# Kernel tuning notes

Hardware: AMD Instinct MI355X
Metric: run time of the kernel (lower is better)

Reference implementation:

```python
import jax, jax.numpy as jnp
import numpy as np

NE, NR, D, H, L = 200000, 500, 128, 4, 2
HD = D // H
N, E, B = 32768, 262144, 256
MARGIN = 1.0


def setup_inputs() -> dict:
    key = jax.random.key(0)
    ks = jax.random.split(key, 16)
    nrm = lambda k, shp, s=0.05: jax.random.normal(k, shp, jnp.float32) * s
    inp = {
        'ent_emb': nrm(ks[0], (NE, D)),
        'rel_emb': nrm(ks[1], (NR, D)),
        'rel_prior': nrm(ks[2], (NR, 1)),
    }
    for i, nm in enumerate(['Wq', 'Wk', 'Wv', 'Wo', 'Wek', 'Wev']):
        inp[nm] = nrm(ks[3 + i], (L, D, D))
    for gi, g in enumerate(['h', 't', 'n']):
        kb = jax.random.fold_in(key, 100 + gi)
        k1, k2, k3, k4 = jax.random.split(kb, 4)
        inp[f'x_{g}'] = jax.random.randint(k1, (N,), 0, NE, jnp.int32)
        inp[f'ei_{g}'] = jax.random.randint(k2, (2, E), 0, N, jnp.int32)
        inp[f'ea_{g}'] = jax.random.randint(k3, (E,), 0, NR, jnp.int32)
        inp[f'y_{g}'] = jax.random.randint(k4, (B,), 0, N // B, jnp.int32)
        inp[f's_{g}'] = jnp.full((B,), N // B, dtype=jnp.int32)
    inp['sample'] = jax.random.randint(ks[9], (B, 3), 0, NR, jnp.int32)
    return inp


def gnn_embed(ent_emb, rel_emb, rel_prior, Wq, Wk, Wv, Wo, Wek, Wev, x, ei, ea, y, s):
    n = x.shape[0]
    h = ent_emb[x]                    # [N, D] node features (embedding lookup)
    e_emb = rel_emb[ea]               # [E, D] edge relation embedding
    e_pri = rel_prior[ea]             # [E, 1] scalar relation prior gate
    src, dst = ei[0], ei[1]
    scale = 1.0 / np.sqrt(HD).astype(np.float32)
    for l in range(L):
        q = (h @ Wq[l]).reshape(n, H, HD)[dst]                               # [E,H,HD]
        k = (h @ Wk[l]).reshape(n, H, HD)[src] + (e_emb @ Wek[l]).reshape(-1, H, HD)
        v = (h @ Wv[l]).reshape(n, H, HD)[src] + (e_emb @ Wev[l]).reshape(-1, H, HD)
        score = jnp.sum(q * k, axis=-1) * scale * e_pri                      # [E,H]
        # segment softmax over incoming edges of each destination node
        m = jax.ops.segment_max(score, dst, num_segments=n)
        m = jnp.where(jnp.isfinite(m), m, 0.0)
        ex = jnp.exp(score - m[dst])
        den = jax.ops.segment_sum(ex, dst, num_segments=n)[dst]
        alpha = ex / (den + 1e-16)                                           # [E,H]
        msg = jax.ops.segment_sum((alpha[..., None] * v).reshape(-1, D), dst, num_segments=n)
        h = jax.nn.gelu(h + msg @ Wo[l])                                     # residual + activation
    # get_real_index: exclusive cumsum of graph sizes + local target index
    offsets = jnp.concatenate([jnp.zeros((1,), s.dtype), jnp.cumsum(s)[:-1]])
    return h[offsets + y]             # [B, D]


def reference(ent_emb, rel_emb, rel_prior, Wq, Wk, Wv, Wo, Wek, Wev,
              x_h, ei_h, ea_h, y_h, s_h,
              x_t, ei_t, ea_t, y_t, s_t,
              x_n, ei_n, ea_n, y_n, s_n, sample):
    g = lambda x, ei, ea, y, s: gnn_embed(ent_emb, rel_emb, rel_prior, Wq, Wk, Wv, Wo, Wek, Wev, x, ei, ea, y, s)
    h = g(x_h, ei_h, ea_h, y_h, s_h)[:, None, :]   # [B,1,D]
    t = g(x_t, ei_t, ea_t, y_t, s_t)[:, None, :]
    tn = g(x_n, ei_n, ea_n, y_n, s_n)[:, None, :]
    r = rel_emb[sample[:, 1]][:, None, :]          # [B,1,D]
    proj_t = h + r                                 # TransE projection
    pos = jnp.linalg.norm(t - proj_t + 1e-8, axis=2)   # [B,1]
    negs = jnp.linalg.norm(t - tn + 1e-8, axis=2)      # [B,1]
    neg = jnp.mean(negs, axis=-1)                      # [B]
    # MarginRankingLoss(pos, neg, target=-1): mean(max(0, (pos-neg)+margin)); broadcasts [B,1]-[B] -> [B,B]
    loss = jnp.mean(jnp.maximum(pos - neg + MARGIN, 0.0))
    return loss
```

## Files before the change

kernel.cpp:

```cpp
#include <hip/hip_runtime.h>
#include <hip/hip_bf16.h>
#include <math.h>

#define NEC 200000
#define NRC 500
#define DD 128
#define LLC 2
#define NNODE 32768
#define EEDGE 262144
#define BBATCH 256
#define NG 3
#define BCAP 32
#define NSB 32
#define EPG (EEDGE / NSB)
#define CNTW (NNODE / 4)

typedef __attribute__((ext_vector_type(8))) short short8;
typedef __attribute__((ext_vector_type(4))) float floatx4;
typedef __attribute__((ext_vector_type(2))) float floatx2;

__device__ __forceinline__ float bf2f(unsigned short u) {
  union { unsigned int i; float f; } c; c.i = ((unsigned int)u) << 16; return c.f;
}
__device__ __forceinline__ unsigned short f2bf(float f) {
  union { float f; unsigned int i; } c; c.f = f;
  unsigned int x = c.i;
  unsigned int r = x + 0x7fffu + ((x >> 16) & 1u);
  return (unsigned short)(r >> 16);
}
__device__ __forceinline__ float bfu_lo(unsigned int u) {
  union { unsigned int i; float f; } c; c.i = u << 16; return c.f;
}
__device__ __forceinline__ float bfu_hi(unsigned int u) {
  union { unsigned int i; float f; } c; c.i = u & 0xffff0000u; return c.f;
}

__device__ __forceinline__ bool detect_fm(const void* ent) {
  unsigned int u = ((const unsigned int*)ent)[threadIdx.x & 63];
  bool big = fabsf(bfu_lo(u)) > 100.f;
  return __ballot(big) != 0ull;
}

__global__ __launch_bounds__(128) void k_prep(const void* ent, const void* rel,
    const void* prior, const void* Wq, const void* Wk, const void* Wv, const void* Wo,
    const void* Wek, const void* Wev,
    float* pris, unsigned short* WT, unsigned short* relk, unsigned short* relv) {
  bool fm = detect_fm(ent);
  int bid = blockIdx.x, tid = threadIdx.x;
  if (bid < 4) {
    int r = bid * 128 + tid;
    if (r < NRC) {
      float p = fm ? ((const float*)prior)[r] : bf2f(((const unsigned short*)prior)[r]);
      pris[r] = p * 0.17677669529663687f;
    }
  } else if (bid < 1028) {
    int t = (bid - 4) * 128 + tid;
    int mat = t >> 15;
    int rem = t & 32767;
    int l = rem >> 14;
    int p = rem & 16383;
    int d = p >> 7, c = p & 127;
    const void* W = mat == 0 ? Wq : (mat == 1 ? Wk : (mat == 2 ? Wv : Wo));
    size_t src = (size_t)l * DD * DD + (size_t)c * DD + d;
    float v = fm ? ((const float*)W)[src] : bf2f(((const unsigned short*)W)[src]);
    WT[(((size_t)mat * LLC + l) * DD + d) * DD + c] = f2bf(v);
  } else {
    int rid = bid - 1028;
    int which = rid / 1000;
    int l = (rid / 500) % 2;
    int r = rid % 500;
    int d = tid;
    size_t wofs = (size_t)l * DD * DD;
    const float* Wf = (const float*)(which ? Wev : Wek) + wofs;
    const unsigned short* Wb = (const unsigned short*)(which ? Wev : Wek) + wofs;
    __shared__ float re[DD];
    re[d] = fm ? ((const float*)rel)[r * DD + d] : bf2f(((const unsigned short*)rel)[r * DD + d]);
    __syncthreads();
    float acc = 0.f;
    if (fm) { for (int c = 0; c < DD; ++c) acc += re[c] * Wf[c * DD + d]; }
    else    { for (int c = 0; c < DD; ++c) acc += re[c] * bf2f(Wb[c * DD + d]); }
    unsigned short* out = which ? relv : relk;
    out[((size_t)l * NRC + r) * DD + d] = f2bf(acc);
  }
}

__global__ __launch_bounds__(256) void k_gather(const void* ent,
    const int* x0, const int* x1, const int* x2, unsigned short* hbf) {
  bool fm = detect_fm(ent);
  int bid = blockIdx.x, tid = threadIdx.x;
  int rbase = bid * 64;
  int g = rbase >> 15;
  const int* x = g == 0 ? x0 : (g == 1 ? x1 : x2);
  int c = tid & 31;
  int j8 = tid >> 5;
  int rows[8], xs[8];
  #pragma unroll
  for (int k = 0; k < 8; ++k) {
    rows[k] = rbase + j8 + 8 * k;
    xs[k] = x[rows[k] & (NNODE - 1)];
  }
  if (fm) {
    float4 v[8];
    #pragma unroll
    for (int k = 0; k < 8; ++k)
      v[k] = *reinterpret_cast<const float4*>((const float*)ent + (size_t)xs[k] * DD + c * 4);
    #pragma unroll
    for (int k = 0; k < 8; ++k) {
      uint2 o;
      o.x = ((unsigned int)f2bf(v[k].y) << 16) | (unsigned int)f2bf(v[k].x);
      o.y = ((unsigned int)f2bf(v[k].w) << 16) | (unsigned int)f2bf(v[k].z);
      *reinterpret_cast<uint2*>(hbf + (size_t)rows[k] * DD + c * 4) = o;
    }
  } else {
    uint2 v[8];
    #pragma unroll
    for (int k = 0; k < 8; ++k)
      v[k] = *reinterpret_cast<const uint2*>((const unsigned short*)ent + (size_t)xs[k] * DD + c * 4);
    #pragma unroll
    for (int k = 0; k < 8; ++k)
      *reinterpret_cast<uint2*>(hbf + (size_t)rows[k] * DD + c * 4) = v[k];
  }
}

__global__ __launch_bounds__(1024) void k_count(const int* ei0, const int* ei1,
    const int* ei2, unsigned int* cntw) {
  __shared__ unsigned int cnt[CNTW];
  int bid = blockIdx.x, tid = threadIdx.x;
  int g = bid / NSB, grp = bid % NSB;
  const int* ei = g == 0 ? ei0 : (g == 1 ? ei1 : ei2);
  #pragma unroll
  for (int i = 0; i < CNTW / 1024; ++i) cnt[i * 1024 + tid] = 0u;
  __syncthreads();
  int e0 = grp * EPG;
  #pragma unroll
  for (int i = 0; i < EPG / 1024; ++i) {
    int dst = ei[EEDGE + e0 + i * 1024 + tid];
    atomicAdd(&cnt[dst >> 2], 1u << ((dst & 3) * 8));
  }
  __syncthreads();
  unsigned int* out = cntw + (size_t)(g * NSB + grp) * CNTW;
  #pragma unroll
  for (int i = 0; i < CNTW / 1024; ++i) out[i * 1024 + tid] = cnt[i * 1024 + tid];
}

__global__ __launch_bounds__(256) void k_prefix(const unsigned int* cntw,
    unsigned int* basew, int* deg) {
  int flat = blockIdx.x * 256 + threadIdx.x;
  int g = flat / CNTW, wi = flat % CNTW;
  unsigned int r0 = 0, r1 = 0, r2 = 0, r3 = 0;
  for (int grp = 0; grp < NSB; ++grp) {
    size_t idx = (size_t)(g * NSB + grp) * CNTW + wi;
    unsigned int w = cntw[idx];
    basew[idx] = r0 | (r1 << 8) | (r2 << 16) | (r3 << 24);
    r0 += w & 255u; r1 += (w >> 8) & 255u; r2 += (w >> 16) & 255u; r3 += (w >> 24) & 255u;
  }
  int4 dv = {(int)r0, (int)r1, (int)r2, (int)r3};
  *reinterpret_cast<int4*>(deg + (size_t)g * NNODE + wi * 4) = dv;
}

__global__ __launch_bounds__(1024) void k_place(const int* ei0, const int* ei1,
    const int* ei2, const int* ea0, const int* ea1, const int* ea2,
    const unsigned int* basew, unsigned int* bucket) {
  __shared__ unsigned int cnt[CNTW];
  __shared__ unsigned int basel[CNTW];
  int bid = blockIdx.x, tid = threadIdx.x;
  int g = bid / NSB, grp = bid % NSB;
  const int* ei = g == 0 ? ei0 : (g == 1 ? ei1 : ei2);
  const int* ea = g == 0 ? ea0 : (g == 1 ? ea1 : ea2);
  const unsigned int* brow = basew + (size_t)(g * NSB + grp) * CNTW;
  #pragma unroll
  for (int i = 0; i < CNTW / 1024; ++i) {
    cnt[i * 1024 + tid] = 0u;
    basel[i * 1024 + tid] = brow[i * 1024 + tid];
  }
  __syncthreads();
  int e0 = grp * EPG;
  size_t gb = (size_t)g * NNODE;
  #pragma unroll
  for (int i = 0; i < EPG / 1024; ++i) {
    int e = e0 + i * 1024 + tid;
    int dst = ei[EEDGE + e];
    unsigned int src = (unsigned int)ei[e];
    unsigned int r = (unsigned int)ea[e];
    int sh = (dst & 3) * 8;
    unsigned int old = atomicAdd(&cnt[dst >> 2], 1u << sh);
    unsigned int lpos = (old >> sh) & 255u;
    unsigned int b = (basel[dst >> 2] >> sh) & 255u;
    unsigned int slot = b + lpos;
    if (slot < BCAP)
      bucket[(gb + dst) * BCAP + slot] = src | (r << 15);
  }
}

__device__ __forceinline__ void stage_wt(const unsigned short* WT, int tid,
                                         unsigned short (*Wt)[136]) {
  #pragma unroll
  for (int pass = 0; pass < 8; ++pass) {
    int idx = pass * 256 + tid;
    int d = idx >> 4, c0 = (idx & 15) << 3;
    *reinterpret_cast<short8*>(&Wt[d][c0]) =
        *reinterpret_cast<const short8*>(WT + d * DD + c0);
  }
}

__global__ __launch_bounds__(256) void k_gemm_qkv(const unsigned short* A,
    const unsigned short* WT, int layer, unsigned short* Qo, unsigned char* KV) {
  __shared__ unsigned short Wt[DD][136];
  int g = blockIdx.y;
  const unsigned short* Ag = A + (size_t)g * NNODE * DD;
  int tid = threadIdx.x;
  int w = tid >> 6, lane = tid & 63;
  int m = lane & 15, quad = lane >> 4;
  int row = blockIdx.x * 64 + w * 16 + m;
  int rowbase = blockIdx.x * 64;
  const unsigned short* arow = Ag + (size_t)row * DD;
  short8 a[4];
  #pragma unroll
  for (int ks = 0; ks < 4; ++ks)
    a[ks] = *reinterpret_cast<const short8*>(arow + ks * 32 + quad * 8);

  for (int mat = 0; mat < 3; ++mat) {
    if (mat) __syncthreads();
    stage_wt(WT + ((size_t)mat * LLC + layer) * DD * DD, tid, Wt);
    __syncthreads();
    floatx4 acc[8];
    #pragma unroll
    for (int t = 0; t < 8; ++t) acc[t] = (floatx4){0.f, 0.f, 0.f, 0.f};
    #pragma unroll
    for (int ks = 0; ks < 4; ++ks) {
      #pragma unroll
      for (int t = 0; t < 8; ++t) {
        short8 b = *reinterpret_cast<const short8*>(&Wt[t * 16 + m][ks * 32 + quad * 8]);
        acc[t] = __builtin_amdgcn_mfma_f32_16x16x32_bf16(a[ks], b, acc[t], 0, 0, 0);
      }
    }
    __syncthreads();
    unsigned short* ut = &Wt[0][0];
    #pragma unroll
    for (int t = 0; t < 8; ++t) {
      #pragma unroll
      for (int r = 0; r < 4; ++r) {
        ut[(w * 16 + quad * 4 + r) * 136 + t * 16 + m] = f2bf(acc[t][r]);
      }
    }
    __syncthreads();
    if (mat == 0) {
      unsigned short* Og = Qo + (size_t)g * NNODE * DD;
      #pragma unroll
      for (int k = 0; k < 4; ++k) {
        int flat = k * 256 + tid;
        int rw = flat >> 4, c8 = flat & 15;
        short8 v = *reinterpret_cast<const short8*>(ut + rw * 136 + c8 * 8);
        *reinterpret_cast<short8*>(Og + (size_t)(rowbase + rw) * DD + c8 * 8) = v;
      }
    } else {
      unsigned char* kvb = KV + (size_t)g * NNODE * 256 + (mat == 1 ? 0 : 128);
      #pragma unroll
      for (int k = 0; k < 2; ++k) {
        int flat = k * 256 + tid;
        int rw = flat >> 3, c16 = flat & 7;
        const unsigned short* p = ut + rw * 136 + c16 * 16;
        uint4 va = *reinterpret_cast<const uint4*>(p);
        uint4 vb = *reinterpret_cast<const uint4*>(p + 8);
        unsigned int w0 = __builtin_amdgcn_cvt_pk_fp8_f32(bfu_lo(va.x), bfu_hi(va.x), 0u, false);
        w0 = __builtin_amdgcn_cvt_pk_fp8_f32(bfu_lo(va.y), bfu_hi(va.y), w0, true);
        unsigned int w1 = __builtin_amdgcn_cvt_pk_fp8_f32(bfu_lo(va.z), bfu_hi(va.z), 0u, false);
        w1 = __builtin_amdgcn_cvt_pk_fp8_f32(bfu_lo(va.w), bfu_hi(va.w), w1, true);
        unsigned int w2 = __builtin_amdgcn_cvt_pk_fp8_f32(bfu_lo(vb.x), bfu_hi(vb.x), 0u, false);
        w2 = __builtin_amdgcn_cvt_pk_fp8_f32(bfu_lo(vb.y), bfu_hi(vb.y), w2, true);
        unsigned int w3 = __builtin_amdgcn_cvt_pk_fp8_f32(bfu_lo(vb.z), bfu_hi(vb.z), 0u, false);
        w3 = __builtin_amdgcn_cvt_pk_fp8_f32(bfu_lo(vb.w), bfu_hi(vb.w), w3, true);
        uint4 o = {w0, w1, w2, w3};
        *reinterpret_cast<uint4*>(kvb + (size_t)(rowbase + rw) * 256 + c16 * 16) = o;
      }
    }
  }
}

__global__ __launch_bounds__(256) void k_gemm_o(const unsigned short* A,
    const unsigned short* WT, int layer, unsigned short* hbf) {
  __shared__ unsigned short Wt[DD][136];
  int g = blockIdx.y;
  const unsigned short* Ag = A + (size_t)g * NNODE * DD;
  unsigned short* hbg = hbf + (size_t)g * NNODE * DD;
  int tid = threadIdx.x;
  stage_wt(WT + ((size_t)3 * LLC + layer) * DD * DD, tid, Wt);
  __syncthreads();
  int w = tid >> 6, lane = tid & 63;
  int m = lane & 15, quad = lane >> 4;
  int row = blockIdx.x * 64 + w * 16 + m;
  floatx4 acc[8];
  #pragma unroll
  for (int t = 0; t < 8; ++t) acc[t] = (floatx4){0.f, 0.f, 0.f, 0.f};
  const unsigned short* arow = Ag + (size_t)row * DD;
  #pragma unroll
  for (int ks = 0; ks < 4; ++ks) {
    short8 a = *reinterpret_cast<const short8*>(arow + ks * 32 + quad * 8);
    #pragma unroll
    for (int t = 0; t < 8; ++t) {
      short8 b = *reinterpret_cast<const short8*>(&Wt[t * 16 + m][ks * 32 + quad * 8]);
      acc[t] = __builtin_amdgcn_mfma_f32_16x16x32_bf16(a, b, acc[t], 0, 0, 0);
    }
  }
  __syncthreads();
  float* ft = (float*)&Wt[0][0];
  #pragma unroll
  for (int t = 0; t < 8; ++t) {
    #pragma unroll
    for (int r = 0; r < 4; ++r) {
      ft[(w * 16 + quad * 4 + r) * 136 + t * 16 + m] = acc[t][r];
    }
  }
  __syncthreads();
  int rowbase = blockIdx.x * 64;
  #pragma unroll
  for (int k = 0; k < 8; ++k) {
    int flat = k * 256 + tid;
    int rw = flat >> 5, c4 = flat & 31;
    float4 v = *reinterpret_cast<const float4*>(ft + rw * 136 + c4 * 4);
    size_t gi = (size_t)(rowbase + rw) * DD + c4 * 4;
    uint2 hv = *reinterpret_cast<const uint2*>(hbg + gi);
    float h0 = bfu_lo(hv.x), h1 = bfu_hi(hv.x), h2 = bfu_lo(hv.y), h3 = bfu_hi(hv.y);
    float r0, r1, r2, r3;
    {
      float xv = v.x + h0;
      float z2 = 1.5957691216057308f * (xv + 0.044715f * xv * xv * xv);
      r0 = xv / (1.f + __expf(-z2));
      xv = v.y + h1;
      z2 = 1.5957691216057308f * (xv + 0.044715f * xv * xv * xv);
      r1 = xv / (1.f + __expf(-z2));
      xv = v.z + h2;
      z2 = 1.5957691216057308f * (xv + 0.044715f * xv * xv * xv);
      r2 = xv / (1.f + __expf(-z2));
      xv = v.w + h3;
      z2 = 1.5957691216057308f * (xv + 0.044715f * xv * xv * xv);
      r3 = xv / (1.f + __expf(-z2));
    }
    uint2 o;
    o.x = ((unsigned int)f2bf(r1) << 16) | (unsigned int)f2bf(r0);
    o.y = ((unsigned int)f2bf(r3) << 16) | (unsigned int)f2bf(r2);
    *reinterpret_cast<uint2*>(hbg + gi) = o;
  }
}

__global__ __launch_bounds__(256) void k_attn(const unsigned short* Q, const unsigned char* KV,
    const unsigned short* relk, const unsigned short* relv,
    const float* pris, const int* deg, const unsigned int* bucket, int layer,
    unsigned short* msgb) {
  int w = threadIdx.x >> 6, lane = threadIdx.x & 63;
  int sq = lane >> 4;
  int sl = lane & 15;
  int g = blockIdx.y;
  int dst = blockIdx.x * 4 + w;
  const unsigned short* rk = relk + (size_t)layer * NRC * DD;
  const unsigned short* rv = relv + (size_t)layer * NRC * DD;
  const unsigned char* KVg = KV + (size_t)g * NNODE * 256;
  size_t gofs = (size_t)g * NNODE * DD;

  uint4 qu = *reinterpret_cast<const uint4*>(Q + gofs + (size_t)dst * DD + sl * 8);
  floatx2 q01 = {bfu_lo(qu.x), bfu_hi(qu.x)};
  floatx2 q23 = {bfu_lo(qu.y), bfu_hi(qu.y)};
  floatx2 q45 = {bfu_lo(qu.z), bfu_hi(qu.z)};
  floatx2 q67 = {bfu_lo(qu.w), bfu_hi(qu.w)};

  float den = 0.f;
  floatx2 m01 = {0.f, 0.f}, m23 = {0.f, 0.f}, m45 = {0.f, 0.f}, m67 = {0.f, 0.f};
  int dg = deg[g * NNODE + dst]; if (dg > BCAP) dg = BCAP;
  size_t base = ((size_t)g * NNODE + dst) * BCAP;
  if (dg > 0) {
    int niter = (dg + 3) >> 2;
    int e1 = 4 + sq; if (e1 >= dg) e1 = dg - 1;
    unsigned int pe_nxt = bucket[base + (sq < dg ? sq : dg - 1)];
    unsigned int pe_fut = bucket[base + e1];
    int src = (int)(pe_nxt & 32767u);
    int r = (int)(pe_nxt >> 15);
    const unsigned char* kvrow = KVg + (size_t)src * 256;
    uint2 k8 = *reinterpret_cast<const uint2*>(kvrow + sl * 8);
    uint2 v8 = *reinterpret_cast<const uint2*>(kvrow + 128 + sl * 8);
    uint4 rku = *reinterpret_cast<const uint4*>(rk + (size_t)r * DD + sl * 8);
    uint4 rvu = *reinterpret_cast<const uint4*>(rv + (size_t)r * DD + sl * 8);
    float p = pris[r];
    pe_nxt = pe_fut;
    for (int i = 0; i < niter; ++i) {
      int ef = 4 * (i + 2) + sq; if (ef >= dg) ef = dg - 1;
      pe_fut = bucket[base + ef];
      int nsrc = (int)(pe_nxt & 32767u);
      int nr = (int)(pe_nxt >> 15);
      const unsigned char* nkv = KVg + (size_t)nsrc * 256;
      uint2 nk8 = *reinterpret_cast<const uint2*>(nkv + sl * 8);
      uint2 nv8 = *reinterpret_cast<const uint2*>(nkv + 128 + sl * 8);
      uint4 nrku = *reinterpret_cast<const uint4*>(rk + (size_t)nr * DD + sl * 8);
      uint4 nrvu = *reinterpret_cast<const uint4*>(rv + (size_t)nr * DD + sl * 8);
      float np = pris[nr];
      floatx2 kk01 = __builtin_amdgcn_cvt_pk_f32_fp8(k8.x, false);
      floatx2 kk23 = __builtin_amdgcn_cvt_pk_f32_fp8(k8.x, true);
      floatx2 kk45 = __builtin_amdgcn_cvt_pk_f32_fp8(k8.y, false);
      floatx2 kk67 = __builtin_amdgcn_cvt_pk_f32_fp8(k8.y, true);
      floatx2 rk01 = {bfu_lo(rku.x), bfu_hi(rku.x)};
      floatx2 rk23 = {bfu_lo(rku.y), bfu_hi(rku.y)};
      floatx2 rk45 = {bfu_lo(rku.z), bfu_hi(rku.z)};
      floatx2 rk67 = {bfu_lo(rku.w), bfu_hi(rku.w)};
      floatx2 sv = (kk01 + rk01) * q01;
      sv += (kk23 + rk23) * q23;
      sv += (kk45 + rk45) * q45;
      sv += (kk67 + rk67) * q67;
      float s = sv.x + sv.y;
      s += __shfl_xor(s, 1); s += __shfl_xor(s, 2);
      bool valid = (4 * i + sq) < dg;
      float ex = valid ? __expf(s * p) : 0.f;
      floatx2 vv01 = __builtin_amdgcn_cvt_pk_f32_fp8(v8.x, false);
      floatx2 vv23 = __builtin_amdgcn_cvt_pk_f32_fp8(v8.x, true);
      floatx2 vv45 = __builtin_amdgcn_cvt_pk_f32_fp8(v8.y, false);
      floatx2 vv67 = __builtin_amdgcn_cvt_pk_f32_fp8(v8.y, true);
      floatx2 rv01 = {bfu_lo(rvu.x), bfu_hi(rvu.x)};
      floatx2 rv23 = {bfu_lo(rvu.y), bfu_hi(rvu.y)};
      floatx2 rv45 = {bfu_lo(rvu.z), bfu_hi(rvu.z)};
      floatx2 rv67 = {bfu_lo(rvu.w), bfu_hi(rvu.w)};
      floatx2 ex2 = {ex, ex};
      den += ex;
      m01 += ex2 * (vv01 + rv01);
      m23 += ex2 * (vv23 + rv23);
      m45 += ex2 * (vv45 + rv45);
      m67 += ex2 * (vv67 + rv67);
      k8 = nk8; v8 = nv8; rku = nrku; rvu = nrvu; p = np;
      pe_nxt = pe_fut;
    }
  }
  den += __shfl_xor(den, 16); den += __shfl_xor(den, 32);
  m01.x += __shfl_xor(m01.x, 16); m01.x += __shfl_xor(m01.x, 32);
  m01.y += __shfl_xor(m01.y, 16); m01.y += __shfl_xor(m01.y, 32);
  m23.x += __shfl_xor(m23.x, 16); m23.x += __shfl_xor(m23.x, 32);
  m23.y += __shfl_xor(m23.y, 16); m23.y += __shfl_xor(m23.y, 32);
  m45.x += __shfl_xor(m45.x, 16); m45.x += __shfl_xor(m45.x, 32);
  m45.y += __shfl_xor(m45.y, 16); m45.y += __shfl_xor(m45.y, 32);
  m67.x += __shfl_xor(m67.x, 16); m67.x += __shfl_xor(m67.x, 32);
  m67.y += __shfl_xor(m67.y, 16); m67.y += __shfl_xor(m67.y, 32);
  float inv = 1.f / (den + 1e-16f);
  if (sq == 0) {
    uint4 o;
    o.x = ((unsigned int)f2bf(m01.y * inv) << 16) | (unsigned int)f2bf(m01.x * inv);
    o.y = ((unsigned int)f2bf(m23.y * inv) << 16) | (unsigned int)f2bf(m23.x * inv);
    o.z = ((unsigned int)f2bf(m45.y * inv) << 16) | (unsigned int)f2bf(m45.x * inv);
    o.w = ((unsigned int)f2bf(m67.y * inv) << 16) | (unsigned int)f2bf(m67.x * inv);
    *reinterpret_cast<uint4*>(msgb + gofs + (size_t)dst * DD + sl * 8) = o;
  }
}

__global__ __launch_bounds__(128) void k_ep(const unsigned short* hbf, const void* ent,
    const void* rel,
    const int* y0, const int* s0, const int* y1, const int* s1, const int* y2, const int* s2,
    const int* sample, float* pos, float* neg) {
  bool fm = detect_fm(ent);
  int b = blockIdx.x, d = threadIdx.x;
  int oh = 0, ot = 0, on = 0;
  for (int j = 0; j < b; ++j) { oh += s0[j]; ot += s1[j]; on += s2[j]; }
  int ih = oh + y0[b], it = ot + y1[b], in_ = on + y2[b];
  float th = bf2f(hbf[((size_t)0 * NNODE + ih) * DD + d]);
  float tt = bf2f(hbf[((size_t)1 * NNODE + it) * DD + d]);
  float tn = bf2f(hbf[((size_t)2 * NNODE + in_) * DD + d]);
  int r = sample[b * 3 + 1];
  float rr = fm ? ((const float*)rel)[r * DD + d] : bf2f(((const unsigned short*)rel)[r * DD + d]);
  float dp = tt - (th + rr) + 1e-8f;
  float dn = tt - tn + 1e-8f;
  float ap = dp * dp, an = dn * dn;
  for (int o = 32; o > 0; o >>= 1) { ap += __shfl_down(ap, o); an += __shfl_down(an, o); }
  __shared__ float sa[2], sb[2];
  if ((d & 63) == 0) { sa[d >> 6] = ap; sb[d >> 6] = an; }
  __syncthreads();
  if (d == 0) { pos[b] = sqrtf(sa[0] + sa[1]); neg[b] = sqrtf(sb[0] + sb[1]); }
}

__global__ __launch_bounds__(256) void k_hinge(const float* pos, const float* neg,
    const void* ent, void* out) {
  bool fm = detect_fm(ent);
  __shared__ float ns[BBATCH];
  __shared__ float wsum[4];
  int t = threadIdx.x;
  ns[t] = neg[t];
  float pb = pos[t];
  __syncthreads();
  float local = 0.f;
  for (int j = 0; j < BBATCH; ++j) {
    float v = pb - ns[j] + 1.0f;
    local += v > 0.f ? v : 0.f;
  }
  for (int o = 32; o > 0; o >>= 1) local += __shfl_down(local, o);
  if ((t & 63) == 0) wsum[t >> 6] = local;
  __syncthreads();
  if (t == 0) {
    float loss = (wsum[0] + wsum[1] + wsum[2] + wsum[3]) * (1.f / (256.f * 256.f));
    if (fm) ((float*)out)[0] = loss;
    else    ((unsigned short*)out)[0] = f2bf(loss);
  }
}

extern "C" void kernel_launch(void* const* d_in, const int* in_sizes, int n_in,
                              void* d_out, int out_size, void* d_ws, size_t ws_size,
                              hipStream_t stream) {
  const void* ent   = d_in[0];
  const void* rel   = d_in[1];
  const void* prior = d_in[2];
  const void* Wq  = d_in[3];
  const void* Wk  = d_in[4];
  const void* Wv  = d_in[5];
  const void* Wo  = d_in[6];
  const void* Wek = d_in[7];
  const void* Wev = d_in[8];
  const int* sample = (const int*)d_in[24];

  size_t off = 0;
  char* basep = (char*)d_ws;
  auto alloc = [&](size_t bytes) -> void* {
    void* r = basep + off;
    off = (off + bytes + 255) & ~(size_t)255;
    return r;
  };
  unsigned short* hbf  = (unsigned short*)alloc((size_t)NG * NNODE * DD * 2);
  unsigned short* Qb   = (unsigned short*)alloc((size_t)NG * NNODE * DD * 2);
  unsigned char*  KV   = (unsigned char*)alloc((size_t)NG * NNODE * 256);
  unsigned short* msgb = (unsigned short*)alloc((size_t)NG * NNODE * DD * 2);
  unsigned short* relk = (unsigned short*)alloc((size_t)LLC * NRC * DD * 2);
  unsigned short* relv = (unsigned short*)alloc((size_t)LLC * NRC * DD * 2);
  unsigned short* WT   = (unsigned short*)alloc((size_t)4 * LLC * DD * DD * 2);
  float* pris = (float*)alloc((size_t)NRC * 4);
  int*   deg  = (int*)alloc((size_t)NG * NNODE * 4);
  unsigned int* bucket = (unsigned int*)alloc((size_t)NG * NNODE * BCAP * 4);
  unsigned int* cntw   = (unsigned int*)alloc((size_t)NG * NSB * CNTW * 4);
  unsigned int* basew  = (unsigned int*)alloc((size_t)NG * NSB * CNTW * 4);
  float* pos  = (float*)alloc((size_t)BBATCH * 4);
  float* neg  = (float*)alloc((size_t)BBATCH * 4);

  const int* x0  = (const int*)d_in[9],  *x1 = (const int*)d_in[14], *x2 = (const int*)d_in[19];
  const int* ei0 = (const int*)d_in[10], *ei1 = (const int*)d_in[15], *ei2 = (const int*)d_in[20];
  const int* ea0 = (const int*)d_in[11], *ea1 = (const int*)d_in[16], *ea2 = (const int*)d_in[21];
  const int* y0  = (const int*)d_in[12], *y1 = (const int*)d_in[17], *y2 = (const int*)d_in[22];
  const int* s0  = (const int*)d_in[13], *s1 = (const int*)d_in[18], *s2 = (const int*)d_in[23];

  k_prep<<<3028, 128, 0, stream>>>(ent, rel, prior, Wq, Wk, Wv, Wo, Wek, Wev,
                                   pris, WT, relk, relv);
  k_gather<<<1536, 256, 0, stream>>>(ent, x0, x1, x2, hbf);
  k_count<<<NG * NSB, 1024, 0, stream>>>(ei0, ei1, ei2, cntw);
  k_prefix<<<NG * CNTW / 256, 256, 0, stream>>>(cntw, basew, deg);
  k_place<<<NG * NSB, 1024, 0, stream>>>(ei0, ei1, ei2, ea0, ea1, ea2, basew, bucket);
  for (int l = 0; l < LLC; ++l) {
    k_gemm_qkv<<<dim3(NNODE / 64, NG), 256, 0, stream>>>(hbf, WT, l, Qb, KV);
    k_attn<<<dim3(NNODE / 4, NG), 256, 0, stream>>>(Qb, KV, relk, relv, pris, deg, bucket, l, msgb);
    k_gemm_o<<<dim3(NNODE / 64, NG), 256, 0, stream>>>(msgb, WT, l, hbf);
  }
  k_ep<<<BBATCH, 128, 0, stream>>>(hbf, ent, rel, y0, s0, y1, s1, y2, s2, sample, pos, neg);
  k_hinge<<<1, BBATCH, 0, stream>>>(pos, neg, ent, d_out);
}
```

Measured before the change: 471.2 us.

## Process two destination nodes per wavefront with deeper gather prefetch in attention

The attention kernel now maps two destination nodes to each 64-lane wavefront (32 lanes each, two edges in flight per node) instead of one node across four edge slots. The grid is halved and the final cross-lane reduction drops one shuffle stage. The KV row prefetch is deepened to two edges ahead, with relation rows loaded one edge ahead. This targets lane waste for low-degree nodes (the average degree is 8) and aims to hide more gather latency. The cost is more loop iterations per node and extra registers for the prefetch pipeline, which may lower occupancy.

```diff
diff --git a/kernel.cpp b/kernel.cpp
--- a/kernel.cpp
+++ b/kernel.cpp
@@ -348,10 +348,11 @@
     const float* pris, const int* deg, const unsigned int* bucket, int layer,
     unsigned short* msgb) {
   int w = threadIdx.x >> 6, lane = threadIdx.x & 63;
-  int sq = lane >> 4;
+  int half = lane >> 5;
+  int hq = (lane >> 4) & 1;
   int sl = lane & 15;
   int g = blockIdx.y;
-  int dst = blockIdx.x * 4 + w;
+  int dst = blockIdx.x * 8 + w * 2 + half;
   const unsigned short* rk = relk + (size_t)layer * NRC * DD;
   const unsigned short* rv = relv + (size_t)layer * NRC * DD;
   const unsigned char* KVg = KV + (size_t)g * NNODE * 256;
@@ -368,75 +369,81 @@
   int dg = deg[g * NNODE + dst]; if (dg > BCAP) dg = BCAP;
   size_t base = ((size_t)g * NNODE + dst) * BCAP;
   if (dg > 0) {
-    int niter = (dg + 3) >> 2;
-    int e1 = 4 + sq; if (e1 >= dg) e1 = dg - 1;
-    unsigned int pe_nxt = bucket[base + (sq < dg ? sq : dg - 1)];
-    unsigned int pe_fut = bucket[base + e1];
-    int src = (int)(pe_nxt & 32767u);
-    int r = (int)(pe_nxt >> 15);
-    const unsigned char* kvrow = KVg + (size_t)src * 256;
-    uint2 k8 = *reinterpret_cast<const uint2*>(kvrow + sl * 8);
-    uint2 v8 = *reinterpret_cast<const uint2*>(kvrow + 128 + sl * 8);
-    uint4 rku = *reinterpret_cast<const uint4*>(rk + (size_t)r * DD + sl * 8);
-    uint4 rvu = *reinterpret_cast<const uint4*>(rv + (size_t)r * DD + sl * 8);
-    float p = pris[r];
-    pe_nxt = pe_fut;
+    int niter = (dg + 1) >> 1;
+    int e0i = hq < dg ? hq : dg - 1;
+    int e1i = 2 + hq; if (e1i >= dg) e1i = dg - 1;
+    int e2i = 4 + hq; if (e2i >= dg) e2i = dg - 1;
+    unsigned int w0 = bucket[base + e0i];
+    unsigned int w1 = bucket[base + e1i];
+    unsigned int w2 = bucket[base + e2i];
+    int sA = (int)(w0 & 32767u), rA = (int)(w0 >> 15);
+    const unsigned char* rowA = KVg + (size_t)sA * 256;
+    uint2 kA = *reinterpret_cast<const uint2*>(rowA + sl * 8);
+    uint2 vA = *reinterpret_cast<const uint2*>(rowA + 128 + sl * 8);
+    uint4 rkA = *reinterpret_cast<const uint4*>(rk + (size_t)rA * DD + sl * 8);
+    uint4 rvA = *reinterpret_cast<const uint4*>(rv + (size_t)rA * DD + sl * 8);
+    float pA = pris[rA];
+    int sB = (int)(w1 & 32767u);
+    const unsigned char* rowB = KVg + (size_t)sB * 256;
+    uint2 kB = *reinterpret_cast<const uint2*>(rowB + sl * 8);
+    uint2 vB = *reinterpret_cast<const uint2*>(rowB + 128 + sl * 8);
     for (int i = 0; i < niter; ++i) {
-      int ef = 4 * (i + 2) + sq; if (ef >= dg) ef = dg - 1;
-      pe_fut = bucket[base + ef];
-      int nsrc = (int)(pe_nxt & 32767u);
-      int nr = (int)(pe_nxt >> 15);
-      const unsigned char* nkv = KVg + (size_t)nsrc * 256;
-      uint2 nk8 = *reinterpret_cast<const uint2*>(nkv + sl * 8);
-      uint2 nv8 = *reinterpret_cast<const uint2*>(nkv + 128 + sl * 8);
-      uint4 nrku = *reinterpret_cast<const uint4*>(rk + (size_t)nr * DD + sl * 8);
-      uint4 nrvu = *reinterpret_cast<const uint4*>(rv + (size_t)nr * DD + sl * 8);
-      float np = pris[nr];
-      floatx2 kk01 = __builtin_amdgcn_cvt_pk_f32_fp8(k8.x, false);
-      floatx2 kk23 = __builtin_amdgcn_cvt_pk_f32_fp8(k8.x, true);
-      floatx2 kk45 = __builtin_amdgcn_cvt_pk_f32_fp8(k8.y, false);
-      floatx2 kk67 = __builtin_amdgcn_cvt_pk_f32_fp8(k8.y, true);
-      floatx2 rk01 = {bfu_lo(rku.x), bfu_hi(rku.x)};
-      floatx2 rk23 = {bfu_lo(rku.y), bfu_hi(rku.y)};
-      floatx2 rk45 = {bfu_lo(rku.z), bfu_hi(rku.z)};
-      floatx2 rk67 = {bfu_lo(rku.w), bfu_hi(rku.w)};
+      int e3 = 2 * (i + 3) + hq; if (e3 >= dg) e3 = dg - 1;
+      unsigned int w3 = bucket[base + e3];
+      int sC = (int)(w2 & 32767u);
+      const unsigned char* rowC = KVg + (size_t)sC * 256;
+      uint2 kC = *reinterpret_cast<const uint2*>(rowC + sl * 8);
+      uint2 vC = *reinterpret_cast<const uint2*>(rowC + 128 + sl * 8);
+      int rB = (int)(w1 >> 15);
+      uint4 rkB = *reinterpret_cast<const uint4*>(rk + (size_t)rB * DD + sl * 8);
+      uint4 rvB = *reinterpret_cast<const uint4*>(rv + (size_t)rB * DD + sl * 8);
+      float pB = pris[rB];
+      floatx2 kk01 = __builtin_amdgcn_cvt_pk_f32_fp8(kA.x, false);
+      floatx2 kk23 = __builtin_amdgcn_cvt_pk_f32_fp8(kA.x, true);
+      floatx2 kk45 = __builtin_amdgcn_cvt_pk_f32_fp8(kA.y, false);
+      floatx2 kk67 = __builtin_amdgcn_cvt_pk_f32_fp8(kA.y, true);
+      floatx2 rk01 = {bfu_lo(rkA.x), bfu_hi(rkA.x)};
+      floatx2 rk23 = {bfu_lo(rkA.y), bfu_hi(rkA.y)};
+      floatx2 rk45 = {bfu_lo(rkA.z), bfu_hi(rkA.z)};
+      floatx2 rk67 = {bfu_lo(rkA.w), bfu_hi(rkA.w)};
       floatx2 sv = (kk01 + rk01) * q01;
       sv += (kk23 + rk23) * q23;
       sv += (kk45 + rk45) * q45;
       sv += (kk67 + rk67) * q67;
       float s = sv.x + sv.y;
       s += __shfl_xor(s, 1); s += __shfl_xor(s, 2);
-      bool valid = (4 * i + sq) < dg;
-      float ex = valid ? __expf(s * p) : 0.f;
-      floatx2 vv01 = __builtin_amdgcn_cvt_pk_f32_fp8(v8.x, false);
-      floatx2 vv23 = __builtin_amdgcn_cvt_pk_f32_fp8(v8.x, true);
-      floatx2 vv45 = __builtin_amdgcn_cvt_pk_f32_fp8(v8.y, false);
-      floatx2 vv67 = __builtin_amdgcn_cvt_pk_f32_fp8(v8.y, true);
-      floatx2 rv01 = {bfu_lo(rvu.x), bfu_hi(rvu.x)};
-      floatx2 rv23 = {bfu_lo(rvu.y), bfu_hi(rvu.y)};
-      floatx2 rv45 = {bfu_lo(rvu.z), bfu_hi(rvu.z)};
-      floatx2 rv67 = {bfu_lo(rvu.w), bfu_hi(rvu.w)};
+      bool valid = (2 * i + hq) < dg;
+      float ex = valid ? __expf(s * pA) : 0.f;
+      floatx2 vv01 = __builtin_amdgcn_cvt_pk_f32_fp8(vA.x, false);
+      floatx2 vv23 = __builtin_amdgcn_cvt_pk_f32_fp8(vA.x, true);
+      floatx2 vv45 = __builtin_amdgcn_cvt_pk_f32_fp8(vA.y, false);
+      floatx2 vv67 = __builtin_amdgcn_cvt_pk_f32_fp8(vA.y, true);
+      floatx2 rv01 = {bfu_lo(rvA.x), bfu_hi(rvA.x)};
+      floatx2 rv23 = {bfu_lo(rvA.y), bfu_hi(rvA.y)};
+      floatx2 rv45 = {bfu_lo(rvA.z), bfu_hi(rvA.z)};
+      floatx2 rv67 = {bfu_lo(rvA.w), bfu_hi(rvA.w)};
       floatx2 ex2 = {ex, ex};
       den += ex;
       m01 += ex2 * (vv01 + rv01);
       m23 += ex2 * (vv23 + rv23);
       m45 += ex2 * (vv45 + rv45);
       m67 += ex2 * (vv67 + rv67);
-      k8 = nk8; v8 = nv8; rku = nrku; rvu = nrvu; p = np;
-      pe_nxt = pe_fut;
-    }
-  }
-  den += __shfl_xor(den, 16); den += __shfl_xor(den, 32);
-  m01.x += __shfl_xor(m01.x, 16); m01.x += __shfl_xor(m01.x, 32);
-  m01.y += __shfl_xor(m01.y, 16); m01.y += __shfl_xor(m01.y, 32);
-  m23.x += __shfl_xor(m23.x, 16); m23.x += __shfl_xor(m23.x, 32);
-  m23.y += __shfl_xor(m23.y, 16); m23.y += __shfl_xor(m23.y, 32);
-  m45.x += __shfl_xor(m45.x, 16); m45.x += __shfl_xor(m45.x, 32);
-  m45.y += __shfl_xor(m45.y, 16); m45.y += __shfl_xor(m45.y, 32);
-  m67.x += __shfl_xor(m67.x, 16); m67.x += __shfl_xor(m67.x, 32);
-  m67.y += __shfl_xor(m67.y, 16); m67.y += __shfl_xor(m67.y, 32);
+      kA = kB; vA = vB; kB = kC; vB = vC;
+      rkA = rkB; rvA = rvB; pA = pB;
+      w1 = w2; w2 = w3;
+    }
+  }
+  den += __shfl_xor(den, 16);
+  m01.x += __shfl_xor(m01.x, 16);
+  m01.y += __shfl_xor(m01.y, 16);
+  m23.x += __shfl_xor(m23.x, 16);
+  m23.y += __shfl_xor(m23.y, 16);
+  m45.x += __shfl_xor(m45.x, 16);
+  m45.y += __shfl_xor(m45.y, 16);
+  m67.x += __shfl_xor(m67.x, 16);
+  m67.y += __shfl_xor(m67.y, 16);
   float inv = 1.f / (den + 1e-16f);
-  if (sq == 0) {
+  if (hq == 0) {
     uint4 o;
     o.x = ((unsigned int)f2bf(m01.y * inv) << 16) | (unsigned int)f2bf(m01.x * inv);
     o.y = ((unsigned int)f2bf(m23.y * inv) << 16) | (unsigned int)f2bf(m23.x * inv);
@@ -544,7 +551,7 @@
   k_place<<<NG * NSB, 1024, 0, stream>>>(ei0, ei1, ei2, ea0, ea1, ea2, basew, bucket);
   for (int l = 0; l < LLC; ++l) {
     k_gemm_qkv<<<dim3(NNODE / 64, NG), 256, 0, stream>>>(hbf, WT, l, Qb, KV);
-    k_attn<<<dim3(NNODE / 4, NG), 256, 0, stream>>>(Qb, KV, relk, relv, pris, deg, bucket, l, msgb);
+    k_attn<<<dim3(NNODE / 8, NG), 256, 0, stream>>>(Qb, KV, relk, relv, pris, deg, bucket, l, msgb);
     k_gemm_o<<<dim3(NNODE / 64, NG), 256, 0, stream>>>(msgb, WT, l, hbf);
   }
   k_ep<<<BBATCH, 128, 0, stream>>>(hbf, ent, rel, y0, s0, y1, s1, y2, s2, sample, pos, neg);
```

New measurement: 476.0 us. Within noise of the previous version (+1.0%).
